# Optimization experiments

Hardware: AMD Instinct MI355X
Metric: run time of the kernel (lower is better)

## Reference

```python
import jax, jax.numpy as jnp
import numpy as np

V, H, HALF, B, L = 32000, 256, 128, 64, 512


def setup_inputs() -> dict:
    key = jax.random.key(0)
    ks = jax.random.split(key, 16)
    s = 0.02
    return {
        "seq": jax.random.randint(ks[0], (B, L), 0, V),
        "embed": jax.random.normal(ks[1], (V, H), jnp.float32) * s,
        "W1": jax.random.normal(ks[2], (H, 2 * H), jnp.float32) * s,
        "b1": jnp.zeros((2 * H,), jnp.float32),
        "W2": jax.random.normal(ks[3], (2 * H, H), jnp.float32) * s,
        "b2": jnp.zeros((H,), jnp.float32),
        "ln_g": jnp.ones((H,), jnp.float32),
        "ln_b": jnp.zeros((H,), jnp.float32),
        "Wsem": jax.random.normal(ks[4], (H, HALF), jnp.float32) * s,
        "bsem": jnp.zeros((HALF,), jnp.float32),
        "Wepi": jax.random.normal(ks[5], (H, HALF), jnp.float32) * s,
        "bepi": jnp.zeros((HALF,), jnp.float32),
        "Wout": jax.random.normal(ks[6], (2 * HALF, V), jnp.float32) * s,
        "bout": jnp.zeros((V,), jnp.float32),
    }


def _encode(seq, embed, W1, b1, W2, b2, ln_g, ln_b):
    e = embed[seq]                                  # [B, L, H]
    ff = jnp.maximum(e @ W1 + b1, 0.0) @ W2 + b2    # [B, L, H]
    x = e + ff
    mu = jnp.mean(x, -1, keepdims=True)
    var = jnp.mean((x - mu) ** 2, -1, keepdims=True)
    return (x - mu) / jnp.sqrt(var + 1e-5) * ln_g + ln_b


def _delta_step(carry, inp):
    M_s, M_e = carry
    ks, ke, scale = inp  # ks/ke: [B, half]; scale scalar
    vps = jnp.einsum("bij,bj->bi", M_s, ks)
    dvs = ks - vps / (jnp.sum(ks * ks, -1, keepdims=True) + 1e-6)
    M_s = M_s + dvs[:, :, None] * ks[:, None, :]
    vpe = jnp.einsum("bij,bj->bi", M_e, ke)
    dve = ke - vpe / (jnp.sum(ke * ke, -1, keepdims=True) + 1e-6)
    M_e = M_e + scale * (dve[:, :, None] * ke[:, None, :])
    return (M_s, M_e), None


def reference(seq, embed, W1, b1, W2, b2, ln_g, ln_b,
              Wsem, bsem, Wepi, bepi, Wout, bout):
    h = _encode(seq, embed, W1, b1, W2, b2, ln_g, ln_b)   # [B, L, H]
    Bs, Ls, _ = h.shape
    half = Wsem.shape[1]
    # keys for all write steps t = 0 .. L-2, precomputed in one GEMM
    ks_all = (h[:, :-1] @ Wsem + bsem).transpose(1, 0, 2)  # [L-1, B, half]
    ke_all = (h[:, :-1] @ Wepi + bepi).transpose(1, 0, 2)
    scales = jnp.arange(1, Ls, dtype=h.dtype) / Ls         # (t+1)/L
    M0 = jnp.zeros((Bs, half, half), h.dtype)
    (M_s, M_e), _ = jax.lax.scan(_delta_step, (M0, M0), (ks_all, ke_all, scales))
    q = h[:, -1, :]
    cs = jnp.einsum("bij,bj->bi", M_s, q @ Wsem + bsem)
    ce = jnp.einsum("bij,bj->bi", M_e, q @ Wepi + bepi)
    return jnp.concatenate([cs, ce], -1) @ Wout + bout     # [B, V]
```

## Files before the change

kernel.cpp:

```cpp
#include <hip/hip_runtime.h>
#include <hip/hip_bf16.h>
#include <stdint.h>

#define B_   64
#define L_   512
#define H_   256
#define H2_  512
#define HALF_ 128
#define V_   32000
#define NTOK_ (B_*L_)

typedef __attribute__((ext_vector_type(8))) short bf16x8;
typedef __attribute__((ext_vector_type(4))) float f32x4;

__device__ __forceinline__ float bf2f(short h){
    union { unsigned u; float f; } v; v.u = ((unsigned)(unsigned short)h) << 16; return v.f;
}
__device__ __forceinline__ short f2bf(float f){
    union { float f; unsigned u; } v; v.f = f;
    unsigned r = v.u + 0x7fffu + ((v.u >> 16) & 1u);
    return (short)(r >> 16);
}

__global__ __launch_bounds__(256) void k_prep(
    const float* __restrict__ W1, const float* __restrict__ W2,
    const float* __restrict__ Wsem, const float* __restrict__ Wepi,
    const float* __restrict__ bsem, const float* __restrict__ bepi,
    short* __restrict__ W1t, short* __restrict__ W2t, short* __restrict__ Wpt,
    float* __restrict__ bp)
{
    const int n = blockIdx.x, t = threadIdx.x;
    if (n < 256) {
        const int k = n;
        W1t[t*256 + k]         = f2bf(W1[k*H2_ + t]);
        W1t[(256 + t)*256 + k] = f2bf(W1[k*H2_ + 256 + t]);
    } else if (n < 768) {
        const int k = n - 256;
        W2t[t*512 + k] = f2bf(W2[k*H_ + t]);
    } else {
        const int k = n - 768;
        float a = (t < 128) ? Wsem[k*HALF_ + t] : Wepi[k*HALF_ + (t-128)];
        Wpt[t*256 + k] = f2bf(a);
        if (k == 0) bp[t] = (t < 128) ? bsem[t] : bepi[t-128];
    }
}

#define EA_LD 264

__global__ __launch_bounds__(512, 4) void k_encode_fused(
    const int* __restrict__ seq, const float* __restrict__ embed,
    const short* __restrict__ W1t, const float* __restrict__ b1,
    const short* __restrict__ W2t, const float* __restrict__ b2,
    const float* __restrict__ ln_g, const float* __restrict__ ln_b,
    const short* __restrict__ Wpt, const float* __restrict__ bp,
    float* __restrict__ kske)
{
    __shared__ __align__(16) short eA[64*EA_LD];
    __shared__ __align__(16) short fB[64*EA_LD];
    __shared__ float2 lnp[8][64];
    __shared__ float2 stat[64];

    const int tid = threadIdx.x;
    const int lo  = tid & 15;
    const int hi  = (tid >> 4) & 3;
    const int wv  = tid >> 6;
    const int n0  = wv * 32;
    const int tokBase = blockIdx.x * 64;
    short* hA = eA;

    bf16x8 g1c0 = *(const bf16x8*)(W1t + ((size_t)(n0 + lo))*256 + 8*hi);
    bf16x8 g1c1 = *(const bf16x8*)(W1t + ((size_t)(n0 + 16 + lo))*256 + 8*hi);

    {
        const int tk = tid >> 3, part = tid & 7;
        const float4* src = (const float4*)(embed + (size_t)seq[tokBase + tk] * H_);
#pragma unroll
        for (int i = 0; i < 8; ++i) {
            float4 v = src[part + 8*i];
            short4 o; o.x = f2bf(v.x); o.y = f2bf(v.y); o.z = f2bf(v.z); o.w = f2bf(v.w);
            *(short4*)&eA[tk*EA_LD + (part + 8*i)*4] = o;
        }
    }
    __syncthreads();

    f32x4 acc2[4][2];
#pragma unroll
    for (int m = 0; m < 4; ++m) { acc2[m][0] = (f32x4){0,0,0,0}; acc2[m][1] = (f32x4){0,0,0,0}; }

#pragma unroll
    for (int h = 0; h < 2; ++h) {
        f32x4 acc1[4][2];
#pragma unroll
        for (int m = 0; m < 4; ++m) { acc1[m][0] = (f32x4){0,0,0,0}; acc1[m][1] = (f32x4){0,0,0,0}; }
        {
            const short* Bb = W1t + ((size_t)(h*256 + n0 + lo))*256;
            bf16x8 bc0, bc1;
            if (h == 0) { bc0 = g1c0; bc1 = g1c1; }
            else {
                bc0 = *(const bf16x8*)(Bb + 8*hi);
                bc1 = *(const bf16x8*)(Bb + 16*256 + 8*hi);
            }
#pragma unroll
            for (int kk = 0; kk < 8; ++kk) {
                const int k0 = kk*32 + 8*hi;
                bf16x8 bn0, bn1;
                if (kk < 7) {
                    bn0 = *(const bf16x8*)(Bb + k0 + 32);
                    bn1 = *(const bf16x8*)(Bb + 16*256 + k0 + 32);
                }
#pragma unroll
                for (int m = 0; m < 4; ++m) {
                    bf16x8 a = *(const bf16x8*)&eA[(lo + 16*m)*EA_LD + k0];
                    acc1[m][0] = __builtin_amdgcn_mfma_f32_16x16x32_bf16(a, bc0, acc1[m][0], 0,0,0);
                    acc1[m][1] = __builtin_amdgcn_mfma_f32_16x16x32_bf16(a, bc1, acc1[m][1], 0,0,0);
                }
                if (kk < 7) { bc0 = bn0; bc1 = bn1; }
            }
        }
        const short* Bb2 = W2t + ((size_t)(n0 + lo))*512 + h*256;
        bf16x8 g2c0 = *(const bf16x8*)(Bb2 + 8*hi);
        bf16x8 g2c1 = *(const bf16x8*)(Bb2 + 16*512 + 8*hi);
        {
            const float bb0 = b1[h*256 + n0 + lo];
            const float bb1 = b1[h*256 + n0 + 16 + lo];
#pragma unroll
            for (int m = 0; m < 4; ++m)
#pragma unroll
                for (int r = 0; r < 4; ++r) {
                    const int row = m*16 + hi*4 + r;
                    fB[row*EA_LD + n0 + lo]      = f2bf(fmaxf(acc1[m][0][r] + bb0, 0.f));
                    fB[row*EA_LD + n0 + 16 + lo] = f2bf(fmaxf(acc1[m][1][r] + bb1, 0.f));
                }
        }
        __syncthreads();
        {
            bf16x8 bc0 = g2c0, bc1 = g2c1;
#pragma unroll
            for (int kk = 0; kk < 8; ++kk) {
                const int k0 = kk*32 + 8*hi;
                bf16x8 bn0, bn1;
                if (kk < 7) {
                    bn0 = *(const bf16x8*)(Bb2 + k0 + 32);
                    bn1 = *(const bf16x8*)(Bb2 + 16*512 + k0 + 32);
                }
#pragma unroll
                for (int m = 0; m < 4; ++m) {
                    bf16x8 a = *(const bf16x8*)&fB[(lo + 16*m)*EA_LD + k0];
                    acc2[m][0] = __builtin_amdgcn_mfma_f32_16x16x32_bf16(a, bc0, acc2[m][0], 0,0,0);
                    acc2[m][1] = __builtin_amdgcn_mfma_f32_16x16x32_bf16(a, bc1, acc2[m][1], 0,0,0);
                }
                if (kk < 7) { bc0 = bn0; bc1 = bn1; }
            }
        }
        __syncthreads();
    }

    const int col0 = n0 + lo, col1 = n0 + 16 + lo;

    {
        const float bb0 = b2[col0], bb1 = b2[col1];
#pragma unroll
        for (int m = 0; m < 4; ++m)
#pragma unroll
            for (int r = 0; r < 4; ++r) {
                const int row = m*16 + hi*4 + r;
                acc2[m][0][r] += bb0 + bf2f(eA[row*EA_LD + col0]);
                acc2[m][1][r] += bb1 + bf2f(eA[row*EA_LD + col1]);
            }
#pragma unroll
        for (int m = 0; m < 4; ++m)
#pragma unroll
            for (int r = 0; r < 4; ++r) {
                float x0 = acc2[m][0][r], x1 = acc2[m][1][r];
                float s  = x0 + x1;
                float s2 = fmaf(x0, x0, x1*x1);
#pragma unroll
                for (int o = 1; o < 16; o <<= 1) { s += __shfl_xor(s, o, 64); s2 += __shfl_xor(s2, o, 64); }
                if (lo == 0) { float2 p; p.x = s; p.y = s2; lnp[wv][m*16 + hi*4 + r] = p; }
            }
    }
    __syncthreads();
    if (tid < 64) {
        float s = 0.f, s2 = 0.f;
#pragma unroll
        for (int w = 0; w < 8; ++w) { float2 p = lnp[w][tid]; s += p.x; s2 += p.y; }
        float mu  = s * (1.f/256.f);
        float var = s2 * (1.f/256.f) - mu*mu;
        float2 st; st.x = mu; st.y = rsqrtf(var + 1e-5f);
        stat[tid] = st;
    }
    __syncthreads();

    const short* Bb3 = Wpt + ((size_t)(n0 + lo))*256;
    bf16x8 g3c0 = *(const bf16x8*)(Bb3 + 8*hi);
    bf16x8 g3c1 = *(const bf16x8*)(Bb3 + 16*256 + 8*hi);

    {
        const float g0 = ln_g[col0], g1 = ln_g[col1];
        const float be0 = ln_b[col0], be1 = ln_b[col1];
#pragma unroll
        for (int m = 0; m < 4; ++m)
#pragma unroll
            for (int r = 0; r < 4; ++r) {
                const int row = m*16 + hi*4 + r;
                float2 st = stat[row];
                hA[row*EA_LD + col0] = f2bf((acc2[m][0][r] - st.x) * st.y * g0 + be0);
                hA[row*EA_LD + col1] = f2bf((acc2[m][1][r] - st.x) * st.y * g1 + be1);
            }
    }
    __syncthreads();

    f32x4 acc3[4][2];
#pragma unroll
    for (int m = 0; m < 4; ++m) { acc3[m][0] = (f32x4){0,0,0,0}; acc3[m][1] = (f32x4){0,0,0,0}; }
    {
        bf16x8 bc0 = g3c0, bc1 = g3c1;
#pragma unroll
        for (int kk = 0; kk < 8; ++kk) {
            const int k0 = kk*32 + 8*hi;
            bf16x8 bn0, bn1;
            if (kk < 7) {
                bn0 = *(const bf16x8*)(Bb3 + k0 + 32);
                bn1 = *(const bf16x8*)(Bb3 + 16*256 + k0 + 32);
            }
#pragma unroll
            for (int m = 0; m < 4; ++m) {
                bf16x8 a = *(const bf16x8*)&hA[(lo + 16*m)*EA_LD + k0];
                acc3[m][0] = __builtin_amdgcn_mfma_f32_16x16x32_bf16(a, bc0, acc3[m][0], 0,0,0);
                acc3[m][1] = __builtin_amdgcn_mfma_f32_16x16x32_bf16(a, bc1, acc3[m][1], 0,0,0);
            }
            if (kk < 7) { bc0 = bn0; bc1 = bn1; }
        }
    }
    {
        const float bp0 = bp[col0], bp1 = bp[col1];
#pragma unroll
        for (int m = 0; m < 4; ++m)
#pragma unroll
            for (int r = 0; r < 4; ++r) {
                const int row = m*16 + hi*4 + r;
                kske[(size_t)(tokBase + row)*256 + col0] = acc3[m][0][r] + bp0;
                kske[(size_t)(tokBase + row)*256 + col1] = acc3[m][1][r] + bp1;
            }
    }
}

#define SCAN_BODY(CC, GA, KXA, KYA, NGA, GB, KXB, KYB, NGB) do {              \
    const int c_ = (CC);                                                      \
    wls[2*l] = w.x; wls[2*l+1] = w.y;                                         \
    float p0=0.f, p1=0.f, p2=0.f, p3=0.f;                                     \
    _Pragma("unroll")                                                         \
    for (int i = 0; i < 8; ++i) {                                             \
        float4 wv2 = *(const float4*)&wls[q*32 + 4*i];                        \
        p0 = fmaf(kq[i].x, wv2.x, p0); p1 = fmaf(kq[i].y, wv2.y, p1);         \
        p2 = fmaf(kq[i].z, wv2.z, p2); p3 = fmaf(kq[i].w, wv2.w, p3);         \
    }                                                                         \
    float bb = (p0 + p1) + (p2 + p3);                                         \
    bb += __shfl_xor(bb, 16, 64);                                             \
    bb += __shfl_xor(bb, 32, 64);                                             \
    if (c_ > 0) {                                                             \
        const float* krow = kb + ((size_t)((c_-1)*16 + lo))*256 + q*32;       \
        _Pragma("unroll")                                                     \
        for (int i = 0; i < 8; ++i) kq[i] = *(const float4*)(krow + 4*i);     \
        const float* gr = &Gs[(c_-1)*256 + lo*16];                            \
        _Pragma("unroll")                                                     \
        for (int i = 0; i < 4; ++i) {                                         \
            float4 gt = *(const float4*)(gr + 4*i);                           \
            GB[4*i]=gt.x; GB[4*i+1]=gt.y; GB[4*i+2]=gt.z; GB[4*i+3]=gt.w;     \
        }                                                                     \
        NGB = gvs[(c_-1)*16 + lo];                                            \
        const float* kdr = kb + ((size_t)((c_-1)*16))*256 + 2*l;              \
        _Pragma("unroll")                                                     \
        for (int j = 0; j < 16; ++j) {                                        \
            float2 kt = *(const float2*)(kdr + (size_t)j*256);                \
            KXB[j] = kt.x; KYB[j] = kt.y;                                     \
        }                                                                     \
    }                                                                         \
    const int tl_ = c_*16 + lo;                                               \
    const float cl_ = chain ? ((tl_ < 511) ? (float)(tl_+1)*(1.f/512.f) : 0.f)\
                            : ((tl_ < 511) ? 1.f : 0.f);                      \
    _Pragma("unroll")                                                         \
    for (int j = 15; j >= 0; --j) {                                           \
        float dj = __int_as_float(__builtin_amdgcn_readlane(__float_as_int(bb), j)); \
        bb = fmaf(dj, GA[j], bb);                                             \
        float tg = NGA * dj;                                                  \
        float tc = cl_ * dj;                                                  \
        float gd = __int_as_float(__builtin_amdgcn_readlane(__float_as_int(tg), j)); \
        float cd = __int_as_float(__builtin_amdgcn_readlane(__float_as_int(tc), j)); \
        w.x = fmaf(gd, KXA[j], w.x);  w.y = fmaf(gd, KYA[j], w.y);            \
        ax  = fmaf(cd, KXA[j], ax);   ay  = fmaf(cd, KYA[j], ay);             \
    }                                                                         \
} while (0)

__global__ __launch_bounds__(256) void k_scan(
    const float* __restrict__ kske, short* __restrict__ chi, short* __restrict__ clo)
{
    __shared__ float Gs[32*256];
    __shared__ float gvs[32*16];
    __shared__ float wls[128];

    const int b = blockIdx.x, chain = blockIdx.y;
    const int tid = threadIdx.x;
    const int wvi = tid >> 6;
    const int l   = tid & 63;
    const int lo  = l & 15, q = l >> 4;
    const float* kb = kske + ((size_t)b*L_)*256 + chain*HALF_;

    for (int cc = 0; cc < 8; ++cc) {
        const int c = wvi*8 + cc;
        const float* rowp = kb + ((size_t)(c*16 + lo))*256 + 8*q;
        bf16x8 ah[4], al[4];
#pragma unroll
        for (int m = 0; m < 4; ++m) {
            float4 v0 = *(const float4*)(rowp + m*32);
            float4 v1 = *(const float4*)(rowp + m*32 + 4);
            float f[8] = {v0.x,v0.y,v0.z,v0.w,v1.x,v1.y,v1.z,v1.w};
#pragma unroll
            for (int i = 0; i < 8; ++i) {
                short hh = f2bf(f[i]);
                ah[m][i] = hh;
                al[m][i] = f2bf(f[i] - bf2f(hh));
            }
        }
        f32x4 g = {0.f,0.f,0.f,0.f};
#pragma unroll
        for (int m = 0; m < 4; ++m) {
            g = __builtin_amdgcn_mfma_f32_16x16x32_bf16(ah[m], ah[m], g, 0,0,0);
            g = __builtin_amdgcn_mfma_f32_16x16x32_bf16(ah[m], al[m], g, 0,0,0);
            g = __builtin_amdgcn_mfma_f32_16x16x32_bf16(al[m], ah[m], g, 0,0,0);
        }
        float cand = (lo & 2) ? ((lo & 1) ? g[3] : g[2]) : ((lo & 1) ? g[1] : g[0]);
        float dval = __shfl(cand, (lo >> 2)*16 + lo, 64);

        const int tcol = c*16 + lo;
        float beta = 1.f / (dval + 1e-6f);
        float gam  = chain ? ((float)(tcol+1) * (1.f/512.f)) * beta : beta;
        if (tcol == 511) gam = 0.f;
#pragma unroll
        for (int r = 0; r < 4; ++r)
            Gs[c*256 + (4*q + r)*16 + lo] = -gam * g[r];
        if (l < 16) gvs[c*16 + lo] = -gam;
    }
    __syncthreads();
    if (wvi != 0) return;

    float2 w = *(const float2*)(kb + (size_t)511*256 + 2*l);
    float ax = 0.f, ay = 0.f;

    float ga[16], kxa[16], kya[16], nga;
    float gb_[16], kxb[16], kyb[16], ngb;
    float4 kq[8];

    {
        const float* krow = kb + ((size_t)(31*16 + lo))*256 + q*32;
#pragma unroll
        for (int i = 0; i < 8; ++i) kq[i] = *(const float4*)(krow + 4*i);
        const float* gr = &Gs[31*256 + lo*16];
#pragma unroll
        for (int i = 0; i < 4; ++i) {
            float4 gt = *(const float4*)(gr + 4*i);
            ga[4*i]=gt.x; ga[4*i+1]=gt.y; ga[4*i+2]=gt.z; ga[4*i+3]=gt.w;
        }
        nga = gvs[31*16 + lo];
        const float* kdr = kb + ((size_t)(31*16))*256 + 2*l;
#pragma unroll
        for (int j = 0; j < 16; ++j) {
            float2 kt = *(const float2*)(kdr + (size_t)j*256);
            kxa[j] = kt.x; kya[j] = kt.y;
        }
    }

    for (int it = 0; it < 16; ++it) {
        SCAN_BODY(31 - 2*it, ga,  kxa, kya, nga, gb_, kxb, kyb, ngb);
        SCAN_BODY(30 - 2*it, gb_, kxb, kyb, ngb, ga,  kxa, kya, nga);
    }

    short2 hv, lv;
    hv.x = f2bf(ax); lv.x = f2bf(ax - bf2f(hv.x));
    hv.y = f2bf(ay); lv.y = f2bf(ay - bf2f(hv.y));
    *(short2*)&chi[b*256 + chain*HALF_ + 2*l] = hv;
    *(short2*)&clo[b*256 + chain*HALF_ + 2*l] = lv;
}

__global__ __launch_bounds__(256) void k_out(
    const short* __restrict__ chi, const short* __restrict__ clo,
    const float* __restrict__ Wout, const float* __restrict__ bout,
    float* __restrict__ out)
{
    __shared__ __align__(16) short ch_s[64*EA_LD];
    __shared__ __align__(16) short cl_s[64*EA_LD];
    const int t  = threadIdx.x;
    const int lo = t & 15;
    const int hi = (t >> 4) & 3;
    const int wv = t >> 6;

    {
        const int4* sh = (const int4*)chi;
        const int4* sl = (const int4*)clo;
#pragma unroll
        for (int i = 0; i < 8; ++i) {
            const int idx = t + 256*i;
            const int row = idx >> 5;
            const int c8  = (idx & 31) * 8;
            *(int4*)&ch_s[row*EA_LD + c8] = sh[idx];
            *(int4*)&cl_s[row*EA_LD + c8] = sl[idx];
        }
    }
    __syncthreads();

    const int colbase = blockIdx.x * 64 + wv * 16;
    f32x4 acc[4];
#pragma unroll
    for (int m = 0; m < 4; ++m) acc[m] = (f32x4){0.f,0.f,0.f,0.f};

#pragma unroll
    for (int kk = 0; kk < 8; ++kk) {
        const int k0 = kk*32 + 8*hi;
        bf16x8 bh, bl;
#pragma unroll
        for (int i = 0; i < 8; ++i) {
            float wf = Wout[(size_t)(k0 + i)*V_ + colbase + lo];
            short wh = f2bf(wf);
            bh[i] = wh;
            bl[i] = f2bf(wf - bf2f(wh));
        }
#pragma unroll
        for (int m = 0; m < 4; ++m) {
            bf16x8 ah = *(const bf16x8*)&ch_s[(m*16 + lo)*EA_LD + k0];
            bf16x8 al = *(const bf16x8*)&cl_s[(m*16 + lo)*EA_LD + k0];
            acc[m] = __builtin_amdgcn_mfma_f32_16x16x32_bf16(ah, bh, acc[m], 0,0,0);
            acc[m] = __builtin_amdgcn_mfma_f32_16x16x32_bf16(ah, bl, acc[m], 0,0,0);
            acc[m] = __builtin_amdgcn_mfma_f32_16x16x32_bf16(al, bh, acc[m], 0,0,0);
        }
    }

    const float bo = bout[colbase + lo];
#pragma unroll
    for (int m = 0; m < 4; ++m)
#pragma unroll
        for (int r = 0; r < 4; ++r)
            out[(size_t)(m*16 + hi*4 + r)*V_ + colbase + lo] = acc[m][r] + bo;
}

extern "C" void kernel_launch(void* const* d_in, const int* in_sizes, int n_in,
                              void* d_out, int out_size, void* d_ws, size_t ws_size,
                              hipStream_t stream)
{
    (void)in_sizes; (void)n_in; (void)out_size; (void)ws_size;
    const int*   seq   = (const int*)  d_in[0];
    const float* embed = (const float*)d_in[1];
    const float* W1    = (const float*)d_in[2];
    const float* b1    = (const float*)d_in[3];
    const float* W2    = (const float*)d_in[4];
    const float* b2    = (const float*)d_in[5];
    const float* ln_g  = (const float*)d_in[6];
    const float* ln_b  = (const float*)d_in[7];
    const float* Wsem  = (const float*)d_in[8];
    const float* bsem  = (const float*)d_in[9];
    const float* Wepi  = (const float*)d_in[10];
    const float* bepi  = (const float*)d_in[11];
    const float* Wout  = (const float*)d_in[12];
    const float* bout  = (const float*)d_in[13];
    float* out = (float*)d_out;

    char* wp = (char*)d_ws;
    short* W1t = (short*)wp;  wp += (size_t)512*256*2;
    short* W2t = (short*)wp;  wp += (size_t)256*512*2;
    short* Wpt = (short*)wp;  wp += (size_t)256*256*2;
    float* bp  = (float*)wp;  wp += 256*4;
    float* kske= (float*)wp;  wp += (size_t)NTOK_*256*4;
    short* chi = (short*)wp;  wp += (size_t)B_*256*2;
    short* clo = (short*)wp;  wp += (size_t)B_*256*2;

    k_prep<<<1024, 256, 0, stream>>>(W1, W2, Wsem, Wepi, bsem, bepi, W1t, W2t, Wpt, bp);
    k_encode_fused<<<NTOK_/64, 512, 0, stream>>>(seq, embed, W1t, b1, W2t, b2,
                                                 ln_g, ln_b, Wpt, bp, kske);
    k_scan<<<dim3(B_, 2), 256, 0, stream>>>(kske, chi, clo);
    k_out<<<V_/64, 256, 0, stream>>>(chi, clo, Wout, bout, out);
}
```

Baseline: 105.8 us.

## Software-pipeline FFN in 128-wide quarters with double-buffered hidden tile

Splits the 512-wide FFN hidden dimension into four 128-wide chunks. GEMM1 for the next chunk is computed while GEMM2 consumes the current chunk from a double-buffered LDS tile, so only one barrier is needed per chunk. The intent is to overlap the two GEMMs, cut the LDS footprint of the hidden tile and lower register pressure. In exchange it adds more barriers overall, and each wave does narrower GEMM1 work with one accumulator column instead of two.

```diff
diff --git a/kernel.cpp b/kernel.cpp
--- a/kernel.cpp
+++ b/kernel.cpp
@@ -46,6 +46,7 @@
 }
 
 #define EA_LD 264
+#define FQ_LD 136
 
 __global__ __launch_bounds__(512, 4) void k_encode_fused(
     const int* __restrict__ seq, const float* __restrict__ embed,
@@ -56,7 +57,7 @@
     float* __restrict__ kske)
 {
     __shared__ __align__(16) short eA[64*EA_LD];
-    __shared__ __align__(16) short fB[64*EA_LD];
+    __shared__ __align__(16) short fBq[2][64*FQ_LD];
     __shared__ float2 lnp[8][64];
     __shared__ float2 stat[64];
 
@@ -65,11 +66,9 @@
     const int hi  = (tid >> 4) & 3;
     const int wv  = tid >> 6;
     const int n0  = wv * 32;
+    const int g1c = wv * 16 + lo;
     const int tokBase = blockIdx.x * 64;
     short* hA = eA;
-
-    bf16x8 g1c0 = *(const bf16x8*)(W1t + ((size_t)(n0 + lo))*256 + 8*hi);
-    bf16x8 g1c1 = *(const bf16x8*)(W1t + ((size_t)(n0 + 16 + lo))*256 + 8*hi);
 
     {
         const int tk = tid >> 3, part = tid & 7;
@@ -87,70 +86,82 @@
 #pragma unroll
     for (int m = 0; m < 4; ++m) { acc2[m][0] = (f32x4){0,0,0,0}; acc2[m][1] = (f32x4){0,0,0,0}; }
 
-#pragma unroll
-    for (int h = 0; h < 2; ++h) {
-        f32x4 acc1[4][2];
-#pragma unroll
-        for (int m = 0; m < 4; ++m) { acc1[m][0] = (f32x4){0,0,0,0}; acc1[m][1] = (f32x4){0,0,0,0}; }
-        {
-            const short* Bb = W1t + ((size_t)(h*256 + n0 + lo))*256;
-            bf16x8 bc0, bc1;
-            if (h == 0) { bc0 = g1c0; bc1 = g1c1; }
-            else {
-                bc0 = *(const bf16x8*)(Bb + 8*hi);
-                bc1 = *(const bf16x8*)(Bb + 16*256 + 8*hi);
-            }
+    {
+        f32x4 acc1[4];
+#pragma unroll
+        for (int m = 0; m < 4; ++m) acc1[m] = (f32x4){0,0,0,0};
+        const short* Bb = W1t + ((size_t)g1c)*256;
+        bf16x8 bc = *(const bf16x8*)(Bb + 8*hi);
+#pragma unroll
+        for (int kk = 0; kk < 8; ++kk) {
+            const int k0 = kk*32 + 8*hi;
+            bf16x8 bn;
+            if (kk < 7) bn = *(const bf16x8*)(Bb + k0 + 32);
+#pragma unroll
+            for (int m = 0; m < 4; ++m) {
+                bf16x8 a = *(const bf16x8*)&eA[(lo + 16*m)*EA_LD + k0];
+                acc1[m] = __builtin_amdgcn_mfma_f32_16x16x32_bf16(a, bc, acc1[m], 0,0,0);
+            }
+            if (kk < 7) bc = bn;
+        }
+        const float bb = b1[g1c];
+#pragma unroll
+        for (int m = 0; m < 4; ++m)
+#pragma unroll
+            for (int r = 0; r < 4; ++r)
+                fBq[0][(m*16 + hi*4 + r)*FQ_LD + g1c] = f2bf(fmaxf(acc1[m][r] + bb, 0.f));
+    }
+    __syncthreads();
+
+#pragma unroll
+    for (int q = 0; q < 4; ++q) {
+        f32x4 accn[4];
+        if (q < 3) {
+#pragma unroll
+            for (int m = 0; m < 4; ++m) accn[m] = (f32x4){0,0,0,0};
+            const short* Bb = W1t + ((size_t)((q+1)*128 + g1c))*256;
+            bf16x8 bc = *(const bf16x8*)(Bb + 8*hi);
 #pragma unroll
             for (int kk = 0; kk < 8; ++kk) {
                 const int k0 = kk*32 + 8*hi;
-                bf16x8 bn0, bn1;
-                if (kk < 7) {
-                    bn0 = *(const bf16x8*)(Bb + k0 + 32);
-                    bn1 = *(const bf16x8*)(Bb + 16*256 + k0 + 32);
-                }
+                bf16x8 bn;
+                if (kk < 7) bn = *(const bf16x8*)(Bb + k0 + 32);
 #pragma unroll
                 for (int m = 0; m < 4; ++m) {
                     bf16x8 a = *(const bf16x8*)&eA[(lo + 16*m)*EA_LD + k0];
-                    acc1[m][0] = __builtin_amdgcn_mfma_f32_16x16x32_bf16(a, bc0, acc1[m][0], 0,0,0);
-                    acc1[m][1] = __builtin_amdgcn_mfma_f32_16x16x32_bf16(a, bc1, acc1[m][1], 0,0,0);
+                    accn[m] = __builtin_amdgcn_mfma_f32_16x16x32_bf16(a, bc, accn[m], 0,0,0);
                 }
-                if (kk < 7) { bc0 = bn0; bc1 = bn1; }
-            }
-        }
-        const short* Bb2 = W2t + ((size_t)(n0 + lo))*512 + h*256;
-        bf16x8 g2c0 = *(const bf16x8*)(Bb2 + 8*hi);
-        bf16x8 g2c1 = *(const bf16x8*)(Bb2 + 16*512 + 8*hi);
+                if (kk < 7) bc = bn;
+            }
+        }
         {
-            const float bb0 = b1[h*256 + n0 + lo];
-            const float bb1 = b1[h*256 + n0 + 16 + lo];
+            const short* Bb2 = W2t + ((size_t)(n0 + lo))*512 + q*128;
+            bf16x8 c0 = *(const bf16x8*)(Bb2 + 8*hi);
+            bf16x8 c1 = *(const bf16x8*)(Bb2 + 16*512 + 8*hi);
+#pragma unroll
+            for (int kk = 0; kk < 4; ++kk) {
+                const int k0 = kk*32 + 8*hi;
+                bf16x8 nb0, nb1;
+                if (kk < 3) {
+                    nb0 = *(const bf16x8*)(Bb2 + k0 + 32);
+                    nb1 = *(const bf16x8*)(Bb2 + 16*512 + k0 + 32);
+                }
+#pragma unroll
+                for (int m = 0; m < 4; ++m) {
+                    bf16x8 a = *(const bf16x8*)&fBq[q & 1][(lo + 16*m)*FQ_LD + k0];
+                    acc2[m][0] = __builtin_amdgcn_mfma_f32_16x16x32_bf16(a, c0, acc2[m][0], 0,0,0);
+                    acc2[m][1] = __builtin_amdgcn_mfma_f32_16x16x32_bf16(a, c1, acc2[m][1], 0,0,0);
+                }
+                if (kk < 3) { c0 = nb0; c1 = nb1; }
+            }
+        }
+        if (q < 3) {
+            const float bb = b1[(q+1)*128 + g1c];
 #pragma unroll
             for (int m = 0; m < 4; ++m)
 #pragma unroll
-                for (int r = 0; r < 4; ++r) {
-                    const int row = m*16 + hi*4 + r;
-                    fB[row*EA_LD + n0 + lo]      = f2bf(fmaxf(acc1[m][0][r] + bb0, 0.f));
-                    fB[row*EA_LD + n0 + 16 + lo] = f2bf(fmaxf(acc1[m][1][r] + bb1, 0.f));
-                }
-        }
-        __syncthreads();
-        {
-            bf16x8 bc0 = g2c0, bc1 = g2c1;
-#pragma unroll
-            for (int kk = 0; kk < 8; ++kk) {
-                const int k0 = kk*32 + 8*hi;
-                bf16x8 bn0, bn1;
-                if (kk < 7) {
-                    bn0 = *(const bf16x8*)(Bb2 + k0 + 32);
-                    bn1 = *(const bf16x8*)(Bb2 + 16*512 + k0 + 32);
-                }
-#pragma unroll
-                for (int m = 0; m < 4; ++m) {
-                    bf16x8 a = *(const bf16x8*)&fB[(lo + 16*m)*EA_LD + k0];
-                    acc2[m][0] = __builtin_amdgcn_mfma_f32_16x16x32_bf16(a, bc0, acc2[m][0], 0,0,0);
-                    acc2[m][1] = __builtin_amdgcn_mfma_f32_16x16x32_bf16(a, bc1, acc2[m][1], 0,0,0);
-                }
-                if (kk < 7) { bc0 = bn0; bc1 = bn1; }
-            }
+                for (int r = 0; r < 4; ++r)
+                    fBq[(q+1) & 1][(m*16 + hi*4 + r)*FQ_LD + g1c] = f2bf(fmaxf(accn[m][r] + bb, 0.f));
         }
         __syncthreads();
     }
@@ -191,10 +202,6 @@
     }
     __syncthreads();
 
-    const short* Bb3 = Wpt + ((size_t)(n0 + lo))*256;
-    bf16x8 g3c0 = *(const bf16x8*)(Bb3 + 8*hi);
-    bf16x8 g3c1 = *(const bf16x8*)(Bb3 + 16*256 + 8*hi);
-
     {
         const float g0 = ln_g[col0], g1 = ln_g[col1];
         const float be0 = ln_b[col0], be1 = ln_b[col1];
@@ -214,14 +221,16 @@
 #pragma unroll
     for (int m = 0; m < 4; ++m) { acc3[m][0] = (f32x4){0,0,0,0}; acc3[m][1] = (f32x4){0,0,0,0}; }
     {
-        bf16x8 bc0 = g3c0, bc1 = g3c1;
+        const short* Bb = Wpt + ((size_t)(n0 + lo))*256;
+        bf16x8 bc0 = *(const bf16x8*)(Bb + 8*hi);
+        bf16x8 bc1 = *(const bf16x8*)(Bb + 16*256 + 8*hi);
 #pragma unroll
         for (int kk = 0; kk < 8; ++kk) {
             const int k0 = kk*32 + 8*hi;
             bf16x8 bn0, bn1;
             if (kk < 7) {
-                bn0 = *(const bf16x8*)(Bb3 + k0 + 32);
-                bn1 = *(const bf16x8*)(Bb3 + 16*256 + k0 + 32);
+                bn0 = *(const bf16x8*)(Bb + k0 + 32);
+                bn1 = *(const bf16x8*)(Bb + 16*256 + k0 + 32);
             }
 #pragma unroll
             for (int m = 0; m < 4; ++m) {
```

Measured after the change: 105.4 us. No clear change (-0.4%).
